# Performance work log

Measured on AMD Instinct MI355X. Metric: run time of the kernel, lower is better.

The kernel has to match this reference:

```python
import jax, jax.numpy as jnp
import numpy as np

SCALE = 100.0  # scale_up in logsumexp_pool


def setup_inputs() -> dict:
    key = jax.random.key(0)
    # NHWC, channels_last
    x = jax.random.normal(key, (8, 256, 256, 64), dtype=jnp.float32)
    return {"x": x}


def reference(x):
    # Faithful to logsumexp_pool: transpose NHWC -> [C,H,W,N], scale by 100,
    # extract 2x2 stride-2 VALID patches (depth axis = 2*2*N after transpose,
    # so the logsumexp reduces over the window AND the batch dim), descale,
    # expand_dims + transpose -> output [1, H/2, W/2, C].
    N, H, W, C = x.shape
    t = jnp.transpose(x, (3, 1, 2, 0)) * SCALE          # [C, H, W, N]
    # stride 2, kernel 2, VALID padding, even H/W -> non-overlapping windows;
    t = t.reshape(C, H // 2, 2, W // 2, 2, N)
    r = jax.nn.logsumexp(t, axis=(2, 4, 5)) * (1.0 / SCALE)  # [C, H/2, W/2]
    return jnp.transpose(r[..., None], (3, 1, 2, 0))    # [1, H/2, W/2, C]
```

## Files before the change

### kernel.cpp

```cpp
#include <hip/hip_runtime.h>


constexpr float SCALE = 100.0f;
constexpr float INV_SCALE = 0.01f;

__device__ inline void chunk_merge(const float4& v0, const float4& v1,
                                   float m[4], float s[4]) {
    const float e0[4] = {v0.x, v0.y, v0.z, v0.w};
    const float e1[4] = {v1.x, v1.y, v1.z, v1.w};
#pragma unroll
    for (int j = 0; j < 4; ++j) {
        const float cm = fmaxf(e0[j], e1[j]);
        const float cs = __expf((e0[j] - cm) * SCALE) + __expf((e1[j] - cm) * SCALE);
        const float mn = fmaxf(m[j], cm);
        s[j] = s[j] * __expf((m[j] - mn) * SCALE) + cs * __expf((cm - mn) * SCALE);
        m[j] = mn;
    }
}

__global__ __launch_bounds__(256) void lse_pool_kernel(const float* __restrict__ x,
                                                       float* __restrict__ out) {
    const int tid = blockIdx.x * 256 + threadIdx.x;
    const int l   = tid & 63;
    const int wv  = tid >> 6;
    const int ho  = wv >> 5;
    const int p0  = (wv & 31) << 3;

    const size_t NS = (size_t)256 * 256 * 64;
    const size_t HS = (size_t)256 * 64;
    const float* base = x + (((size_t)(2 * ho) * 256) + (size_t)p0) * 64 + (size_t)(l * 4);

    float mA[4], sA[4], mB[4], sB[4];
#pragma unroll
    for (int j = 0; j < 4; ++j) { mA[j] = -1e30f; sA[j] = 0.f; mB[j] = -1e30f; sB[j] = 0.f; }

#pragma unroll 2
    for (int n = 0; n < 8; ++n) {
        const float* pn = base + (size_t)n * NS;
        const float4 a0 = *reinterpret_cast<const float4*>(pn);
        const float4 b0 = *reinterpret_cast<const float4*>(pn + 256);
        const float4 a1 = *reinterpret_cast<const float4*>(pn + HS);
        const float4 b1 = *reinterpret_cast<const float4*>(pn + HS + 256);
        chunk_merge(a0, a1, mA, sA);
        chunk_merge(b0, b1, mB, sB);
    }

#pragma unroll
    for (int j = 0; j < 4; ++j) {
        {
            const float m2 = __shfl_xor(mA[j], 16);
            const float s2 = __shfl_xor(sA[j], 16);
            const float mn = fmaxf(mA[j], m2);
            sA[j] = sA[j] * __expf((mA[j] - mn) * SCALE) + s2 * __expf((m2 - mn) * SCALE);
            mA[j] = mn;
        }
        {
            const float m2 = __shfl_xor(mB[j], 16);
            const float s2 = __shfl_xor(sB[j], 16);
            const float mn = fmaxf(mB[j], m2);
            sB[j] = sB[j] * __expf((mB[j] - mn) * SCALE) + s2 * __expf((m2 - mn) * SCALE);
            mB[j] = mn;
        }
    }

    if ((l & 16) == 0) {
        float4 rA, rB;
        rA.x = mA[0] + __logf(sA[0]) * INV_SCALE;
        rA.y = mA[1] + __logf(sA[1]) * INV_SCALE;
        rA.z = mA[2] + __logf(sA[2]) * INV_SCALE;
        rA.w = mA[3] + __logf(sA[3]) * INV_SCALE;
        rB.x = mB[0] + __logf(sB[0]) * INV_SCALE;
        rB.y = mB[1] + __logf(sB[1]) * INV_SCALE;
        rB.z = mB[2] + __logf(sB[2]) * INV_SCALE;
        rB.w = mB[3] + __logf(sB[3]) * INV_SCALE;

        const int c  = (l & 15) << 2;
        const int wo = (p0 >> 1) + (l >> 5);
        const size_t o = ((size_t)ho * 128 + (size_t)wo) * 64 + (size_t)c;
        *reinterpret_cast<float4*>(out + o)            = rA;
        *reinterpret_cast<float4*>(out + o + 2 * 64)   = rB;
    }
}

extern "C" void kernel_launch(void* const* d_in, const int* in_sizes, int n_in,
                              void* d_out, int out_size, void* d_ws, size_t ws_size,
                              hipStream_t stream) {
    const float* x = (const float*)d_in[0];
    float* out = (float*)d_out;
    lse_pool_kernel<<<1024, 256, 0, stream>>>(x, out);
}
```

Before: 185.6 us.

## Split batch reduction across two wave halves and merge via LDS

Each block now covers 16 pixel columns with four waves. Two of the waves reduce batch 0-3 and the other two reduce batch 4-7, and the partial max/sum pairs are combined through shared memory after a barrier. The grid doubles to 2048 blocks so that twice as many waves are in flight, which gives more memory-level parallelism for this bandwidth-bound kernel. The cost is an LDS round trip, a __syncthreads, and half of the waves sitting idle during the final merge and store.

After: 190.0 us. 1.02x slower.

```diff
diff --git a/kernel.cpp b/kernel.cpp
--- a/kernel.cpp
+++ b/kernel.cpp
@@ -3,6 +3,12 @@
 
 constexpr float SCALE = 100.0f;
 constexpr float INV_SCALE = 0.01f;
+
+__device__ inline void pair_merge(float& m, float& s, float m2, float s2) {
+    const float mn = fmaxf(m, m2);
+    s = s * __expf((m - mn) * SCALE) + s2 * __expf((m2 - mn) * SCALE);
+    m = mn;
+}
 
 __device__ inline void chunk_merge(const float4& v0, const float4& v1,
                                    float m[4], float s[4]) {
@@ -12,30 +18,31 @@
     for (int j = 0; j < 4; ++j) {
         const float cm = fmaxf(e0[j], e1[j]);
         const float cs = __expf((e0[j] - cm) * SCALE) + __expf((e1[j] - cm) * SCALE);
-        const float mn = fmaxf(m[j], cm);
-        s[j] = s[j] * __expf((m[j] - mn) * SCALE) + cs * __expf((cm - mn) * SCALE);
-        m[j] = mn;
+        pair_merge(m[j], s[j], cm, cs);
     }
 }
 
 __global__ __launch_bounds__(256) void lse_pool_kernel(const float* __restrict__ x,
                                                        float* __restrict__ out) {
-    const int tid = blockIdx.x * 256 + threadIdx.x;
-    const int l   = tid & 63;
-    const int wv  = tid >> 6;
-    const int ho  = wv >> 5;
-    const int p0  = (wv & 31) << 3;
+    const int t    = threadIdx.x;
+    const int l    = t & 63;
+    const int w    = t >> 6;
+    const int g    = w & 1;
+    const int half = w >> 1;
+    const int ho   = blockIdx.x >> 4;
+    const int p0   = ((blockIdx.x & 15) << 4) + (g << 3);
 
     const size_t NS = (size_t)256 * 256 * 64;
     const size_t HS = (size_t)256 * 64;
-    const float* base = x + (((size_t)(2 * ho) * 256) + (size_t)p0) * 64 + (size_t)(l * 4);
+    const float* base = x + (((size_t)(2 * ho) * 256) + (size_t)p0) * 64
+                          + (size_t)(half * 4) * NS + (size_t)(l * 4);
 
     float mA[4], sA[4], mB[4], sB[4];
 #pragma unroll
     for (int j = 0; j < 4; ++j) { mA[j] = -1e30f; sA[j] = 0.f; mB[j] = -1e30f; sB[j] = 0.f; }
 
 #pragma unroll 2
-    for (int n = 0; n < 8; ++n) {
+    for (int n = 0; n < 4; ++n) {
         const float* pn = base + (size_t)n * NS;
         const float4 a0 = *reinterpret_cast<const float4*>(pn);
         const float4 b0 = *reinterpret_cast<const float4*>(pn + 256);
@@ -47,23 +54,28 @@
 
 #pragma unroll
     for (int j = 0; j < 4; ++j) {
-        {
-            const float m2 = __shfl_xor(mA[j], 16);
-            const float s2 = __shfl_xor(sA[j], 16);
-            const float mn = fmaxf(mA[j], m2);
-            sA[j] = sA[j] * __expf((mA[j] - mn) * SCALE) + s2 * __expf((m2 - mn) * SCALE);
-            mA[j] = mn;
-        }
-        {
-            const float m2 = __shfl_xor(mB[j], 16);
-            const float s2 = __shfl_xor(sB[j], 16);
-            const float mn = fmaxf(mB[j], m2);
-            sB[j] = sB[j] * __expf((mB[j] - mn) * SCALE) + s2 * __expf((m2 - mn) * SCALE);
-            mB[j] = mn;
+        pair_merge(mA[j], sA[j], __shfl_xor(mA[j], 16), __shfl_xor(sA[j], 16));
+        pair_merge(mB[j], sB[j], __shfl_xor(mB[j], 16), __shfl_xor(sB[j], 16));
+    }
+
+    __shared__ float lds[2][64][17];
+    if (half == 1) {
+#pragma unroll
+        for (int j = 0; j < 4; ++j) {
+            lds[g][l][j]      = mA[j];
+            lds[g][l][4 + j]  = sA[j];
+            lds[g][l][8 + j]  = mB[j];
+            lds[g][l][12 + j] = sB[j];
         }
     }
+    __syncthreads();
 
-    if ((l & 16) == 0) {
+    if (half == 0 && (l & 16) == 0) {
+#pragma unroll
+        for (int j = 0; j < 4; ++j) {
+            pair_merge(mA[j], sA[j], lds[g][l][j],     lds[g][l][4 + j]);
+            pair_merge(mB[j], sB[j], lds[g][l][8 + j], lds[g][l][12 + j]);
+        }
         float4 rA, rB;
         rA.x = mA[0] + __logf(sA[0]) * INV_SCALE;
         rA.y = mA[1] + __logf(sA[1]) * INV_SCALE;
@@ -77,8 +89,8 @@
         const int c  = (l & 15) << 2;
         const int wo = (p0 >> 1) + (l >> 5);
         const size_t o = ((size_t)ho * 128 + (size_t)wo) * 64 + (size_t)c;
-        *reinterpret_cast<float4*>(out + o)            = rA;
-        *reinterpret_cast<float4*>(out + o + 2 * 64)   = rB;
+        *reinterpret_cast<float4*>(out + o)       = rA;
+        *reinterpret_cast<float4*>(out + o + 128) = rB;
     }
 }
 
@@ -87,5 +99,5 @@
                               hipStream_t stream) {
     const float* x = (const float*)d_in[0];
     float* out = (float*)d_out;
-    lse_pool_kernel<<<1024, 256, 0, stream>>>(x, out);
+    lse_pool_kernel<<<2048, 256, 0, stream>>>(x, out);
 }
```
